# Kernel tuning notes

Measured on AMD Instinct MI355X. Metric: run time of the kernel, lower is better.

The kernel has to match this reference:

```python
import jax, jax.numpy as jnp
import numpy as np

TOPK = 2
SCALE = 32.0 / 16.0  # alpha / rank
EPS = 1e-20


def setup_inputs() -> dict:
    key = jax.random.key(0)
    ks = jax.random.split(key, 6)
    B, S, D = 4, 4096, 2048
    E, R, QO, VO = 8, 16, 2048, 2048
    return {
        "hidden_states": jax.random.normal(ks[0], (B, S, D), dtype=jnp.float32),
        "router_weight": jax.random.normal(ks[1], (E, D), dtype=jnp.float32) * 0.02,
        "q_lora_a": jax.random.normal(ks[2], (E, D, R), dtype=jnp.float32) * 0.02,
        "q_lora_b": jax.random.normal(ks[3], (E, R, QO), dtype=jnp.float32) * 0.02,
        "v_lora_a": jax.random.normal(ks[4], (E, D, R), dtype=jnp.float32) * 0.02,
        "v_lora_b": jax.random.normal(ks[5], (E, R, VO), dtype=jnp.float32) * 0.02,
    }


def reference(hidden_states, router_weight, q_lora_a, q_lora_b, v_lora_a, v_lora_b):
    orig_shape = hidden_states.shape[:-1]
    D = hidden_states.shape[-1]
    E = router_weight.shape[0]
    h = hidden_states.reshape(-1, D)                       # [T, D]

    # --- routing ---
    logits = h @ router_weight.T                           # [T, E]
    probs = jax.nn.softmax(logits, axis=-1)
    scores, idx = jax.lax.top_k(probs, TOPK)               # [T, K]
    scores = scores / (jnp.sum(scores, axis=-1, keepdims=True) + EPS)
    # dense per-expert combine weight (0 for unselected experts), incl. LoRA scale
    w = jnp.sum(jax.nn.one_hot(idx, E, dtype=h.dtype) * scores[..., None], axis=1) * SCALE  # [T, E]

    # --- grouped LoRA (dense over experts; E and rank are small) ---
    q_low = jnp.einsum('td,edr->ter', h, q_lora_a) * w[:, :, None]  # [T, E, R]
    v_low = jnp.einsum('td,edr->ter', h, v_lora_a) * w[:, :, None]
    q_delta = jnp.einsum('ter,erq->tq', q_low, q_lora_b)            # [T, QO]
    v_delta = jnp.einsum('ter,erv->tv', v_low, v_lora_b)            # [T, VO]

    return (q_delta.reshape(*orig_shape, q_delta.shape[-1]),
            v_delta.reshape(*orig_shape, v_delta.shape[-1]))
```

## Files before the change

kernel.cpp:

```cpp
#include <hip/hip_runtime.h>

#define T_TOKENS 16384
#define DIM 2048
#define NE 8
#define QOUT 2048
#define LSCALE 2.0f

typedef __attribute__((ext_vector_type(4))) float f32x4;
typedef __attribute__((ext_vector_type(8))) short s16x8;
typedef __attribute__((ext_vector_type(4))) short s16x4;

__device__ __forceinline__ short f2bf(float f) {
  unsigned u = __builtin_bit_cast(unsigned, f);
  u += 0x7fffu + ((u >> 16) & 1u);
  return (short)(u >> 16);
}

__device__ __forceinline__ void barrier_lds() {
  asm volatile("s_waitcnt lgkmcnt(0)" ::: "memory");
  __builtin_amdgcn_s_barrier();
}

__global__ __launch_bounds__(256) void k_pack(
    const float* __restrict__ qa, const float* __restrict__ qb,
    const float* __restrict__ va, const float* __restrict__ vb,
    short* __restrict__ Bq1, short* __restrict__ Bv1,
    short* __restrict__ Bq2, short* __restrict__ Bv2) {
  int tid = blockIdx.x * 256 + threadIdx.x;
  if (tid < 65536) {
    int mat = tid >> 15;
    int idx = tid & 32767;
    int d8 = idx >> 7, c = idx & 127;
    int e = c >> 4, r = c & 15;
    const float* src = mat ? va : qa;
    short* dst = mat ? Bv1 : Bq1;
    s16x8 v;
#pragma unroll
    for (int j = 0; j < 8; ++j)
      v[j] = f2bf(src[((size_t)e * DIM + d8 * 8 + j) * 16 + r]);
    *(s16x8*)(dst + (size_t)idx * 8) = v;
  } else {
    int t2 = tid - 65536;
    int mat = t2 >> 15;
    int idx = t2 & 32767;
    int k8 = idx >> 11, c = idx & 2047;
    const float* src = mat ? vb : qb;
    short* dst = mat ? Bv2 : Bq2;
    s16x8 v;
#pragma unroll
    for (int j = 0; j < 8; ++j)
      v[j] = f2bf(src[(size_t)(k8 * 8 + j) * QOUT + c]);
    *(s16x8*)(dst + (size_t)idx * 8) = v;
  }
}

__global__ __launch_bounds__(512, 2) void k_fused(
    const float* __restrict__ h, const float* __restrict__ rw,
    const short* __restrict__ Bq1, const short* __restrict__ Bv1,
    const short* __restrict__ Bq2, const short* __restrict__ Bv2,
    float* __restrict__ out) {
  __shared__ short At[2][32][72];
  __shared__ short low[32][264];
  __shared__ float wl[32][NE];

  const int tid = threadIdx.x;
  const int lane = tid & 63, wv = tid >> 6;
  const int lrow = lane & 15, lk = lane >> 4;
  const int row0 = blockIdx.x * 32;
  const int r  = tid >> 4;
  const int kq = (tid & 15) * 4;
  const int tq = wv >> 2, cq = wv & 3;

  const float* hrow = h + (size_t)(row0 + r) * DIM + kq;
  const short* B1 = (cq >= 2) ? Bv1 : Bq1;
  int cc4[4];
#pragma unroll
  for (int ct = 0; ct < 4; ++ct) cc4[ct] = (cq & 1) * 64 + ct * 16 + lrow;

  float4 hv0 = *(const float4*)(hrow);
  float4 hv1 = *(const float4*)(hrow + 64);

  float lg[NE] = {0.f, 0.f, 0.f, 0.f, 0.f, 0.f, 0.f, 0.f};
  f32x4 acc1[4] = {};

  for (int kb = 0; kb < DIM; kb += 64) {
    const int cur = (kb >> 6) & 1;
    float4 hv2 = *(const float4*)(hrow + ((kb + 128) & (DIM - 1)));
    s16x8 bA[4], bB[4];
#pragma unroll
    for (int ct = 0; ct < 4; ++ct) {
      int d8 = (kb >> 3) + lk;
      bA[ct] = *(const s16x8*)(B1 + ((size_t)d8 * 128 + cc4[ct]) * 8);
      bB[ct] = *(const s16x8*)(B1 + ((size_t)(d8 + 4) * 128 + cc4[ct]) * 8);
    }
    s16x4 hb4;
    hb4[0] = f2bf(hv0.x); hb4[1] = f2bf(hv0.y);
    hb4[2] = f2bf(hv0.z); hb4[3] = f2bf(hv0.w);
    *(s16x4*)&At[cur][r][kq] = hb4;
#pragma unroll
    for (int e = 0; e < NE; ++e) {
      float4 rv = *(const float4*)(rw + e * DIM + kb + kq);
      lg[e] += hv0.x * rv.x + hv0.y * rv.y + hv0.z * rv.z + hv0.w * rv.w;
    }
    barrier_lds();
    s16x8 a0 = *(const s16x8*)&At[cur][tq * 16 + lrow][lk * 8];
    s16x8 a1 = *(const s16x8*)&At[cur][tq * 16 + lrow][32 + lk * 8];
#pragma unroll
    for (int ct = 0; ct < 4; ++ct)
      acc1[ct] = __builtin_amdgcn_mfma_f32_16x16x32_bf16(bA[ct], a0, acc1[ct], 0, 0, 0);
#pragma unroll
    for (int ct = 0; ct < 4; ++ct)
      acc1[ct] = __builtin_amdgcn_mfma_f32_16x16x32_bf16(bB[ct], a1, acc1[ct], 0, 0, 0);
    hv0 = hv1; hv1 = hv2;
  }

#pragma unroll
  for (int e = 0; e < NE; ++e) {
    lg[e] += __shfl_xor(lg[e], 1, 64);
    lg[e] += __shfl_xor(lg[e], 2, 64);
    lg[e] += __shfl_xor(lg[e], 4, 64);
    lg[e] += __shfl_xor(lg[e], 8, 64);
  }
  float mx = lg[0];
#pragma unroll
  for (int e = 1; e < NE; ++e) mx = fmaxf(mx, lg[e]);
  float p[NE], sum = 0.f;
#pragma unroll
  for (int e = 0; e < NE; ++e) { p[e] = expf(lg[e] - mx); sum += p[e]; }
  int i1 = 0; float v1 = p[0];
#pragma unroll
  for (int e = 1; e < NE; ++e) if (p[e] > v1) { v1 = p[e]; i1 = e; }
  float v2 = -1.f; int i2 = 0;
#pragma unroll
  for (int e = 0; e < NE; ++e) if (e != i1 && p[e] > v2) { v2 = p[e]; i2 = e; }
  float s1 = v1 / sum, s2 = v2 / sum;
  float dn = s1 + s2 + 1e-20f;
  float w1 = s1 / dn * LSCALE, w2 = s2 / dn * LSCALE;
  if ((tid & 15) < 8) {
    int el = tid & 7;
    wl[r][el] = (el == i1) ? w1 : ((el == i2) ? w2 : 0.f);
  }

  const int m = wv >> 2;
  const int cwave = (wv & 3) * 512;
  const short* B2 = m ? Bv2 : Bq2;
  s16x8 bc[4];
#pragma unroll
  for (int ct = 0; ct < 4; ++ct) {
    int c = cwave + ct * 16 + lrow;
    bc[ct] = *(const s16x8*)(B2 + ((size_t)lk * QOUT + c) * 8);
  }

  __syncthreads();
  float wgt[4];
#pragma unroll
  for (int ct = 0; ct < 4; ++ct) wgt[ct] = wl[tq * 16 + lrow][(cq & 1) * 4 + ct];
#pragma unroll
  for (int ct = 0; ct < 4; ++ct) {
    s16x4 v;
#pragma unroll
    for (int j = 0; j < 4; ++j) v[j] = f2bf(acc1[ct][j] * wgt[ct]);
    *(s16x4*)&low[tq * 16 + lrow][cq * 64 + ct * 16 + lk * 4] = v;
  }
  barrier_lds();

  float* op = out + (size_t)m * T_TOKENS * QOUT;
  s16x8 a2[2][4];
#pragma unroll
  for (int rt = 0; rt < 2; ++rt)
#pragma unroll
    for (int kk = 0; kk < 4; ++kk)
      a2[rt][kk] = *(const s16x8*)&low[rt * 16 + lrow][m * 128 + kk * 32 + lk * 8];

  f32x4 acc[2][4] = {};
#pragma unroll
  for (int it = 0; it < 32; ++it) {
    const int sub = it >> 2, kk = it & 3;
    const int itn = (it + 1) & 31;
    const int subn = itn >> 2, kkn = itn & 3;
    s16x8 bn[4];
#pragma unroll
    for (int ct = 0; ct < 4; ++ct) {
      int c = cwave + subn * 64 + ct * 16 + lrow;
      bn[ct] = *(const s16x8*)(B2 + ((size_t)(kkn * 4 + lk) * QOUT + c) * 8);
    }
#pragma unroll
    for (int rt = 0; rt < 2; ++rt)
#pragma unroll
      for (int ct = 0; ct < 4; ++ct)
        acc[rt][ct] = __builtin_amdgcn_mfma_f32_16x16x32_bf16(bc[ct], a2[rt][kk], acc[rt][ct], 0, 0, 0);
    if (kk == 3) {
      int cb = cwave + sub * 64;
#pragma unroll
      for (int rt = 0; rt < 2; ++rt)
#pragma unroll
        for (int ct = 0; ct < 4; ++ct) {
          int t = row0 + rt * 16 + lrow;
          int col = cb + ct * 16 + lk * 4;
          __builtin_nontemporal_store(acc[rt][ct], (f32x4*)(op + (size_t)t * QOUT + col));
          acc[rt][ct] = (f32x4){0.f, 0.f, 0.f, 0.f};
        }
    }
#pragma unroll
    for (int ct = 0; ct < 4; ++ct) bc[ct] = bn[ct];
  }
}

extern "C" void kernel_launch(void* const* d_in, const int* in_sizes, int n_in,
                              void* d_out, int out_size, void* d_ws, size_t ws_size,
                              hipStream_t stream) {
  const float* h  = (const float*)d_in[0];
  const float* rw = (const float*)d_in[1];
  const float* qa = (const float*)d_in[2];
  const float* qb = (const float*)d_in[3];
  const float* va = (const float*)d_in[4];
  const float* vb = (const float*)d_in[5];
  float* out = (float*)d_out;
  char* ws = (char*)d_ws;

  short* Bq1 = (short*)(ws);
  short* Bv1 = (short*)(ws + (512 << 10));
  short* Bq2 = (short*)(ws + (1024 << 10));
  short* Bv2 = (short*)(ws + (1536 << 10));

  k_pack<<<512, 256, 0, stream>>>(qa, qb, va, vb, Bq1, Bv1, Bq2, Bv2);
  k_fused<<<T_TOKENS / 32, 512, 0, stream>>>(h, rw, Bq1, Bv1, Bq2, Bv2, out);
}
```

Baseline: 143.3 us.

## Load hidden states directly into MFMA operand registers, dropping LDS staging

The first-stage loop now has each lane load its MFMA A-fragment straight from global memory and convert it to bf16 in registers. This replaces the shared-memory tile and the per-iteration barrier. Router logits are split so each wave computes two experts per token, then exchanged through a small LDS array. Each wave recomputes the softmax and top-k locally, which removes the wl table and one sync. The change also drops the occupancy hint from launch_bounds and reduces unrolling of the second-stage loop, trading possible uncoalesced global reads and redundant h loads across the four column waves for fewer barriers.

```diff
diff --git a/kernel.cpp b/kernel.cpp
--- a/kernel.cpp
+++ b/kernel.cpp
@@ -14,6 +14,13 @@
   unsigned u = __builtin_bit_cast(unsigned, f);
   u += 0x7fffu + ((u >> 16) & 1u);
   return (short)(u >> 16);
+}
+
+__device__ __forceinline__ s16x8 pack8(float4 a, float4 b) {
+  s16x8 r;
+  r[0] = f2bf(a.x); r[1] = f2bf(a.y); r[2] = f2bf(a.z); r[3] = f2bf(a.w);
+  r[4] = f2bf(b.x); r[5] = f2bf(b.y); r[6] = f2bf(b.z); r[7] = f2bf(b.w);
+  return r;
 }
 
 __device__ __forceinline__ void barrier_lds() {
@@ -54,79 +61,85 @@
   }
 }
 
-__global__ __launch_bounds__(512, 2) void k_fused(
+__global__ __launch_bounds__(512) void k_fused(
     const float* __restrict__ h, const float* __restrict__ rw,
     const short* __restrict__ Bq1, const short* __restrict__ Bv1,
     const short* __restrict__ Bq2, const short* __restrict__ Bv2,
     float* __restrict__ out) {
-  __shared__ short At[2][32][72];
+  __shared__ float wraw[32][NE];
   __shared__ short low[32][264];
-  __shared__ float wl[32][NE];
 
   const int tid = threadIdx.x;
   const int lane = tid & 63, wv = tid >> 6;
   const int lrow = lane & 15, lk = lane >> 4;
   const int row0 = blockIdx.x * 32;
-  const int r  = tid >> 4;
-  const int kq = (tid & 15) * 4;
-  const int tq = wv >> 2, cq = wv & 3;
-
-  const float* hrow = h + (size_t)(row0 + r) * DIM + kq;
-  const short* B1 = (cq >= 2) ? Bv1 : Bq1;
-  int cc4[4];
-#pragma unroll
-  for (int ct = 0; ct < 4; ++ct) cc4[ct] = (cq & 1) * 64 + ct * 16 + lrow;
-
-  float4 hv0 = *(const float4*)(hrow);
-  float4 hv1 = *(const float4*)(hrow + 64);
-
-  float lg[NE] = {0.f, 0.f, 0.f, 0.f, 0.f, 0.f, 0.f, 0.f};
+  const int th = wv >> 2;
+  const int colq = wv & 3;
+  const int tok = th * 16 + lrow;
+
+  const float* hl = h + (size_t)(row0 + tok) * DIM + lk * 8;
+  const short* B1 = (colq >= 2) ? Bv1 : Bq1;
+  const int e0 = colq * 2;
+  const float* rwl0 = rw + (size_t)e0 * DIM + lk * 8;
+  const float* rwl1 = rwl0 + DIM;
+  int cc[4];
+#pragma unroll
+  for (int ct = 0; ct < 4; ++ct) cc[ct] = (colq & 1) * 64 + ct * 16 + lrow;
+
+  float lg0 = 0.f, lg1 = 0.f;
   f32x4 acc1[4] = {};
 
-  for (int kb = 0; kb < DIM; kb += 64) {
-    const int cur = (kb >> 6) & 1;
-    float4 hv2 = *(const float4*)(hrow + ((kb + 128) & (DIM - 1)));
-    s16x8 bA[4], bB[4];
-#pragma unroll
-    for (int ct = 0; ct < 4; ++ct) {
-      int d8 = (kb >> 3) + lk;
-      bA[ct] = *(const s16x8*)(B1 + ((size_t)d8 * 128 + cc4[ct]) * 8);
-      bB[ct] = *(const s16x8*)(B1 + ((size_t)(d8 + 4) * 128 + cc4[ct]) * 8);
-    }
-    s16x4 hb4;
-    hb4[0] = f2bf(hv0.x); hb4[1] = f2bf(hv0.y);
-    hb4[2] = f2bf(hv0.z); hb4[3] = f2bf(hv0.w);
-    *(s16x4*)&At[cur][r][kq] = hb4;
-#pragma unroll
-    for (int e = 0; e < NE; ++e) {
-      float4 rv = *(const float4*)(rw + e * DIM + kb + kq);
-      lg[e] += hv0.x * rv.x + hv0.y * rv.y + hv0.z * rv.z + hv0.w * rv.w;
-    }
-    barrier_lds();
-    s16x8 a0 = *(const s16x8*)&At[cur][tq * 16 + lrow][lk * 8];
-    s16x8 a1 = *(const s16x8*)&At[cur][tq * 16 + lrow][32 + lk * 8];
+#pragma unroll 2
+  for (int kb = 0; kb < DIM; kb += 32) {
+    float4 h0 = *(const float4*)(hl + kb);
+    float4 h1 = *(const float4*)(hl + kb + 4);
+    s16x8 b[4];
+    const int d8 = (kb >> 3) + lk;
 #pragma unroll
     for (int ct = 0; ct < 4; ++ct)
-      acc1[ct] = __builtin_amdgcn_mfma_f32_16x16x32_bf16(bA[ct], a0, acc1[ct], 0, 0, 0);
+      b[ct] = *(const s16x8*)(B1 + ((size_t)d8 * 128 + cc[ct]) * 8);
+    float4 r0 = *(const float4*)(rwl0 + kb);
+    float4 r1 = *(const float4*)(rwl0 + kb + 4);
+    float4 r2 = *(const float4*)(rwl1 + kb);
+    float4 r3 = *(const float4*)(rwl1 + kb + 4);
+    lg0 += h0.x * r0.x + h0.y * r0.y + h0.z * r0.z + h0.w * r0.w
+         + h1.x * r1.x + h1.y * r1.y + h1.z * r1.z + h1.w * r1.w;
+    lg1 += h0.x * r2.x + h0.y * r2.y + h0.z * r2.z + h0.w * r2.w
+         + h1.x * r3.x + h1.y * r3.y + h1.z * r3.z + h1.w * r3.w;
+    s16x8 a = pack8(h0, h1);
 #pragma unroll
     for (int ct = 0; ct < 4; ++ct)
-      acc1[ct] = __builtin_amdgcn_mfma_f32_16x16x32_bf16(bB[ct], a1, acc1[ct], 0, 0, 0);
-    hv0 = hv1; hv1 = hv2;
-  }
-
-#pragma unroll
-  for (int e = 0; e < NE; ++e) {
-    lg[e] += __shfl_xor(lg[e], 1, 64);
-    lg[e] += __shfl_xor(lg[e], 2, 64);
-    lg[e] += __shfl_xor(lg[e], 4, 64);
-    lg[e] += __shfl_xor(lg[e], 8, 64);
-  }
-  float mx = lg[0];
-#pragma unroll
-  for (int e = 1; e < NE; ++e) mx = fmaxf(mx, lg[e]);
+      acc1[ct] = __builtin_amdgcn_mfma_f32_16x16x32_bf16(b[ct], a, acc1[ct], 0, 0, 0);
+  }
+
+  lg0 += __shfl_xor(lg0, 16, 64); lg0 += __shfl_xor(lg0, 32, 64);
+  lg1 += __shfl_xor(lg1, 16, 64); lg1 += __shfl_xor(lg1, 32, 64);
+  if (lk == 0) wraw[tok][e0] = lg0;
+  if (lk == 1) wraw[tok][e0 + 1] = lg1;
+
+  const int m = wv >> 2;
+  const int cwave = (wv & 3) * 512;
+  const short* B2 = m ? Bv2 : Bq2;
+  s16x8 bc[4];
+#pragma unroll
+  for (int ct = 0; ct < 4; ++ct) {
+    int c = cwave + ct * 16 + lrow;
+    bc[ct] = *(const s16x8*)(B2 + ((size_t)lk * QOUT + c) * 8);
+  }
+
+  barrier_lds();
+
   float p[NE], sum = 0.f;
-#pragma unroll
-  for (int e = 0; e < NE; ++e) { p[e] = expf(lg[e] - mx); sum += p[e]; }
+  {
+    float l[NE];
+#pragma unroll
+    for (int e = 0; e < NE; ++e) l[e] = wraw[tok][e];
+    float mx = l[0];
+#pragma unroll
+    for (int e = 1; e < NE; ++e) mx = fmaxf(mx, l[e]);
+#pragma unroll
+    for (int e = 0; e < NE; ++e) { p[e] = expf(l[e] - mx); sum += p[e]; }
+  }
   int i1 = 0; float v1 = p[0];
 #pragma unroll
   for (int e = 1; e < NE; ++e) if (p[e] > v1) { v1 = p[e]; i1 = e; }
@@ -136,31 +149,15 @@
   float s1 = v1 / sum, s2 = v2 / sum;
   float dn = s1 + s2 + 1e-20f;
   float w1 = s1 / dn * LSCALE, w2 = s2 / dn * LSCALE;
-  if ((tid & 15) < 8) {
-    int el = tid & 7;
-    wl[r][el] = (el == i1) ? w1 : ((el == i2) ? w2 : 0.f);
-  }
-
-  const int m = wv >> 2;
-  const int cwave = (wv & 3) * 512;
-  const short* B2 = m ? Bv2 : Bq2;
-  s16x8 bc[4];
+
 #pragma unroll
   for (int ct = 0; ct < 4; ++ct) {
-    int c = cwave + ct * 16 + lrow;
-    bc[ct] = *(const s16x8*)(B2 + ((size_t)lk * QOUT + c) * 8);
-  }
-
-  __syncthreads();
-  float wgt[4];
-#pragma unroll
-  for (int ct = 0; ct < 4; ++ct) wgt[ct] = wl[tq * 16 + lrow][(cq & 1) * 4 + ct];
-#pragma unroll
-  for (int ct = 0; ct < 4; ++ct) {
+    int e = (colq & 1) * 4 + ct;
+    float wgt = (e == i1) ? w1 : ((e == i2) ? w2 : 0.f);
     s16x4 v;
 #pragma unroll
-    for (int j = 0; j < 4; ++j) v[j] = f2bf(acc1[ct][j] * wgt[ct]);
-    *(s16x4*)&low[tq * 16 + lrow][cq * 64 + ct * 16 + lk * 4] = v;
+    for (int j = 0; j < 4; ++j) v[j] = f2bf(acc1[ct][j] * wgt);
+    *(s16x4*)&low[tok][colq * 64 + ct * 16 + lk * 4] = v;
   }
   barrier_lds();
 
@@ -173,7 +170,7 @@
       a2[rt][kk] = *(const s16x8*)&low[rt * 16 + lrow][m * 128 + kk * 32 + lk * 8];
 
   f32x4 acc[2][4] = {};
-#pragma unroll
+#pragma unroll 4
   for (int it = 0; it < 32; ++it) {
     const int sub = it >> 2, kk = it & 3;
     const int itn = (it + 1) & 31;
```

New measurement: 195.8 us. 1.37x slower.
